# Performance work log

Measured on AMD Instinct MI355X. Metric: run time of the kernel, lower is better.

The kernel has to match this reference:

```python
import jax, jax.numpy as jnp
import numpy as np

B, N, C, H, DFF = 64, 196, 384, 8, 1536
PATCH = 14              # N == PATCH*PATCH, PATCH = image_size // 2
HD = C // H
SCALE = HD ** -0.5


def setup_inputs() -> dict:
    key = jax.random.key(0)
    ks = jax.random.split(key, 12)
    r = lambda i, shape: jax.random.normal(ks[i], shape, jnp.float32) * 0.02
    return dict(
        src=jax.random.normal(ks[0], (B, N, C), jnp.float32),
        src1=jax.random.normal(ks[1], (B, N, C), jnp.float32),
        ln_pre_g=jnp.ones((C,), jnp.float32), ln_pre_b=jnp.zeros((C,), jnp.float32),
        ln1_g=jnp.ones((C,), jnp.float32), ln1_b=jnp.zeros((C,), jnp.float32),
        wqkv_a=r(2, (C, 4 * C)), wproj_a=r(3, (C, C)), bproj_a=jnp.zeros((C,), jnp.float32),
        se_w1=r(4, (C, C // 16)), se_w2=r(5, (C // 16, C)),
        sa_w=r(6, (1, 2, 5, 5)), sa_b=jnp.zeros((1,), jnp.float32),
        wqkv_c=r(7, (C, 4 * C)), wproj_c=r(8, (C, C)), bproj_c=jnp.zeros((C,), jnp.float32),
        w1=r(9, (C, DFF)), b1=jnp.zeros((DFF,), jnp.float32),
        w2=r(10, (DFF, C)), b2=jnp.zeros((C,), jnp.float32),
    )


def _ln(x, g, b):
    m = x.mean(-1, keepdims=True)
    v = ((x - m) ** 2).mean(-1, keepdims=True)
    return (x - m) * jax.lax.rsqrt(v + 1e-5) * g + b


def _qkv4(x, w):
    b, n, _ = x.shape
    q = (x @ w).reshape(b, n, 4, H, HD).transpose(2, 0, 3, 1, 4)  # (4,B,H,N,hd)
    return q[0], q[1], q[2], q[3]


def _se(q, w1, w2):
    # SELayer: channel gate over (B, H*hd, N)
    b, h, n, c = q.shape
    xt = q.transpose(0, 1, 3, 2).reshape(b, h * c, n)
    fc = lambda v: jax.nn.sigmoid(jax.nn.relu(v @ w1) @ w2)
    gate = fc(xt.mean(-1)) + fc(xt.max(-1))
    xt = xt * gate[:, :, None]
    return xt.reshape(b, h, c, n).transpose(0, 1, 3, 2)


def _sa(q, w, bias):
    # SALayer: spatial gate via 5x5 conv on avg/max channel pooling
    b, h, n, c = q.shape
    xi = q.transpose(0, 1, 3, 2).reshape(b, h * c, PATCH, PATCH)
    pooled = jnp.concatenate([xi.mean(1, keepdims=True), xi.max(1, keepdims=True)], axis=1)
    conv = jax.lax.conv_general_dilated(pooled, w, (1, 1), [(2, 2), (2, 2)],
                                        dimension_numbers=('NCHW', 'OIHW', 'NCHW'))
    gate = jax.nn.sigmoid(conv + bias[None, :, None, None])
    xi = xi * gate
    return xi.reshape(b, h, c, n).transpose(0, 1, 3, 2)


def _merge(o):  # (B,H,N,hd) -> (B,N,C)
    return o.transpose(0, 2, 1, 3).reshape(o.shape[0], o.shape[2], C)


def _attention(x, y, wqkv, wproj, bproj, se_w1, se_w2, sa_w, sa_b):
    qxo, qx, kx, vx = _qkv4(x, wqkv)
    qyo, qy, ky, _ = _qkv4(y, wqkv)
    vy = vx  # original code: vy = qkv[3] (x-stream values)
    qx2 = _se(qx, se_w1, se_w2)
    qy2 = _sa(qy, sa_w, sa_b)
    a1 = jax.nn.softmax(jnp.einsum('bhqd,bhkd->bhqk', qx + qx2, kx) * SCALE, axis=-1)
    a2 = jax.nn.softmax(jnp.einsum('bhqd,bhkd->bhqk', qy + qy2, ky) * SCALE, axis=-1)
    xo = _merge(jnp.einsum('bhqk,bhkd->bhqd', a1, vx)) @ wproj + bproj
    yo = _merge(jnp.einsum('bhqk,bhkd->bhqd', a2, vy)) @ wproj + bproj
    # original overwrites cross outputs with proj(proj(.))
    return xo, yo, xo @ wproj + bproj, yo @ wproj + bproj


def _dif(x, y, wqkv, wproj, bproj):
    qxo, qx, kx, vx = _qkv4(x, wqkv)
    qyo, qy, ky, _ = _qkv4(y, wqkv)
    vy = vx
    a1 = jax.nn.softmax(jnp.einsum('bhqd,bhkd->bhqk', qx, kx) * SCALE, axis=-1)
    a2 = jax.nn.softmax(jnp.einsum('bhqd,bhkd->bhqk', qy, ky) * SCALE, axis=-1)
    ax = jax.nn.softmax(-jnp.einsum('bhqd,bhkd->bhqk', qyo, kx) * SCALE, axis=-1)
    ay = jax.nn.softmax(-jnp.einsum('bhqd,bhkd->bhqk', qxo, ky) * SCALE, axis=-1)
    xo = _merge(jnp.einsum('bhqk,bhkd->bhqd', a1, vx) + jnp.einsum('bhqk,bhkd->bhqd', ax, vx))
    yo = _merge(jnp.einsum('bhqk,bhkd->bhqd', a2, vy) + jnp.einsum('bhqk,bhkd->bhqd', ay, vy))
    return xo @ wproj + bproj, yo @ wproj + bproj


def _mlp(x, w1, b1, w2, b2):
    return jax.nn.gelu(x @ w1 + b1, approximate=False) @ w2 + b2


def reference(src, src1, ln_pre_g, ln_pre_b, ln1_g, ln1_b, wqkv_a, wproj_a, bproj_a,
              se_w1, se_w2, sa_w, sa_b, wqkv_c, wproj_c, bproj_c, w1, b1, w2, b2):
    x0, y0 = src, src1
    xa, ya, xoa, yoa = _attention(_ln(src, ln_pre_g, ln_pre_b), _ln(src1, ln_pre_g, ln_pre_b),
                                  wqkv_a, wproj_a, bproj_a, se_w1, se_w2, sa_w, sa_b)
    x = x0 + xa
    xo = x0 + xoa
    y = y0 + ya
    yo = y0 + yoa
    x, y, xo, yo = (_ln(t, ln1_g, ln1_b) for t in (x, y, xo, yo))
    x = x + _mlp(x, w1, b1, w2, b2)
    y = y + _mlp(y, w1, b1, w2, b2)
    xo = xo + _mlp(xo, w1, b1, w2, b2)
    yo = yo + _mlp(yo, w1, b1, w2, b2)
    # c_attn REPLACES the streams (no residual on attention itself)
    x, y = _dif(_ln(x, ln_pre_g, ln_pre_b), _ln(y, ln_pre_g, ln_pre_b), wqkv_c, wproj_c, bproj_c)
    x = x + _mlp(x, w1, b1, w2, b2)
    y = y + _mlp(y, w1, b1, w2, b2)
    return (x, y, xo, yo)
```

## Files before the change

### kernel.cpp

```cpp
#include <hip/hip_runtime.h>
#include <math.h>

#define Bb   64
#define Nn   196
#define Cc   384
#define Hh   8
#define HDd  48
#define DFFf 1536
#define MRr  (Bb * Nn)

typedef __attribute__((ext_vector_type(8))) short bf16x8v;
typedef __attribute__((ext_vector_type(4))) float f32x4v;

__device__ __forceinline__ ushort f2bf(float f){
  union { float f; uint u; } v; v.f = f;
  uint r = v.u + 0x7FFFu + ((v.u >> 16) & 1u);
  return (ushort)(r >> 16);
}
__device__ __forceinline__ float bf2f(ushort u){
  union { uint u; float f; } v; v.u = ((uint)u) << 16;
  return v.f;
}

__device__ __forceinline__ float wsum(float v){
#pragma unroll
  for (int o = 32; o; o >>= 1) v += __shfl_xor(v, o, 64);
  return v;
}
__device__ __forceinline__ float wmaxr(float v){
#pragma unroll
  for (int o = 32; o; o >>= 1) v = fmaxf(v, __shfl_xor(v, o, 64));
  return v;
}

__global__ void lnstats_k(const float* __restrict__ A, const float* __restrict__ A2,
                          float* __restrict__ m, float* __restrict__ rs){
  int row  = blockIdx.x;
  int lane = threadIdx.x;
  size_t base = (size_t)row * Cc;
  float x[6];
#pragma unroll
  for (int i = 0; i < 6; ++i){
    int c = lane + 64 * i;
    float v = A[base + c];
    if (A2) v += A2[base + c];
    x[i] = v;
  }
  float s = x[0] + x[1] + x[2] + x[3] + x[4] + x[5];
  s = wsum(s);
  float mm = s * (1.f / Cc);
  float vs = 0.f;
#pragma unroll
  for (int i = 0; i < 6; ++i){ float d = x[i] - mm; vs += d * d; }
  vs = wsum(vs);
  if (lane == 0){
    m[row]  = mm;
    rs[row] = rsqrtf(vs * (1.f / Cc) + 1e-5f);
  }
}

__global__ void wconv_k(const float* __restrict__ W, ushort* __restrict__ WT,
                        int K, int N){
  int idx = blockIdx.x * 256 + threadIdx.x;
  if (idx >= K * N) return;
  int k = idx / N, n = idx - k * N;
  WT[(size_t)n * K + k] = f2bf(W[idx]);
}

#define BMm 128
#define BNn 128
#define BKk 64
#define LDK 72

__global__ __launch_bounds__(256) void mgemm_k(
    const float* __restrict__ A, int lda, const float* __restrict__ A2,
    const float* __restrict__ stm, const float* __restrict__ strs,
    const float* __restrict__ ag,  const float* __restrict__ ab,
    const ushort* __restrict__ WT, int ldwt, const float* __restrict__ bias, int act,
    const float* __restrict__ res, int ldres,
    const float* __restrict__ r1, const float* __restrict__ r2,
    const float* __restrict__ rm, const float* __restrict__ rrs,
    const float* __restrict__ rg, const float* __restrict__ rb,
    float* __restrict__ out, int ldo, int M, int K, int N){
  __shared__ ushort As[BMm][LDK];
  __shared__ ushort Bs[BNn][LDK];
  const int tid  = threadIdx.x;
  const int lane = tid & 63;
  const int wid  = tid >> 6;
  const int wr = wid >> 1, wc = wid & 1;
  const int row0 = blockIdx.y * BMm;
  const int n0   = blockIdx.x * BNn;

  f32x4v acc[4][4];
#pragma unroll
  for (int m = 0; m < 4; ++m)
#pragma unroll
    for (int n = 0; n < 4; ++n) acc[m][n] = (f32x4v){0.f, 0.f, 0.f, 0.f};

  const int arow = tid >> 4;
  const int akq  = (tid & 15) * 4;
  const int bcol = tid >> 1;
  const int bko  = (tid & 1) * 32;

  for (int k0 = 0; k0 < K; k0 += BKk){
#pragma unroll
    for (int p = 0; p < 8; ++p){
      int r = arow + p * 16;
      int row = row0 + r;
      int kg = k0 + akq;
      float4 v = *(const float4*)&A[(size_t)row * lda + kg];
      if (A2){
        float4 w = *(const float4*)&A2[(size_t)row * lda + kg];
        v.x += w.x; v.y += w.y; v.z += w.z; v.w += w.w;
      }
      if (stm){
        float mm = stm[row], rr = strs[row];
        float4 g  = *(const float4*)&ag[kg];
        float4 bb = *(const float4*)&ab[kg];
        v.x = (v.x - mm) * rr * g.x + bb.x;
        v.y = (v.y - mm) * rr * g.y + bb.y;
        v.z = (v.z - mm) * rr * g.z + bb.z;
        v.w = (v.w - mm) * rr * g.w + bb.w;
      }
      ushort4 o; o.x = f2bf(v.x); o.y = f2bf(v.y); o.z = f2bf(v.z); o.w = f2bf(v.w);
      *(ushort4*)&As[r][akq] = o;
    }
    {
      const ushort* src = &WT[(size_t)(n0 + bcol) * ldwt + k0 + bko];
#pragma unroll
      for (int q = 0; q < 4; ++q)
        *(uint4*)&Bs[bcol][bko + q * 8] = *(const uint4*)(src + q * 8);
    }
    __syncthreads();
#pragma unroll
    for (int ks = 0; ks < 2; ++ks){
      const int kb = ks * 32 + (lane >> 4) * 8;
      bf16x8v af[4], bfm[4];
#pragma unroll
      for (int m = 0; m < 4; ++m)
        af[m] = *(const bf16x8v*)&As[wr * 64 + m * 16 + (lane & 15)][kb];
#pragma unroll
      for (int n = 0; n < 4; ++n)
        bfm[n] = *(const bf16x8v*)&Bs[wc * 64 + n * 16 + (lane & 15)][kb];
#pragma unroll
      for (int m = 0; m < 4; ++m)
#pragma unroll
        for (int n = 0; n < 4; ++n)
          acc[m][n] = __builtin_amdgcn_mfma_f32_16x16x32_bf16(af[m], bfm[n], acc[m][n], 0, 0, 0);
    }
    __syncthreads();
  }
  const int rbase = row0 + wr * 64 + (lane >> 4) * 4;
  const int cbase = n0 + wc * 64 + (lane & 15);
#pragma unroll
  for (int m = 0; m < 4; ++m){
#pragma unroll
    for (int n = 0; n < 4; ++n){
      int ccol = cbase + n * 16;
      float bv = bias ? bias[ccol] : 0.f;
#pragma unroll
      for (int j = 0; j < 4; ++j){
        int rr_ = rbase + m * 16 + j;
        float v = acc[m][n][j] + bv;
        if (act) v = 0.5f * v * (1.f + erff(v * 0.70710678118654752f));
        if (res) v += res[(size_t)rr_ * ldres + ccol];
        if (r1)  v += (r1[(size_t)rr_ * ldres + ccol] + r2[(size_t)rr_ * ldres + ccol]
                       - rm[rr_]) * rrs[rr_] * rg[ccol] + rb[ccol];
        out[(size_t)rr_ * ldo + ccol] = v;
      }
    }
  }
}

__global__ void se_k(const float* __restrict__ q, int rs_, const float* __restrict__ w1,
                     const float* __restrict__ w2, float* __restrict__ gate){
  int b = blockIdx.x;
  int tid = threadIdx.x;
  __shared__ float mv[Cc], xv[Cc], hid[2][24];
  for (int c = tid; c < Cc; c += 256){
    const float* p = q + (size_t)b * Nn * rs_ + c;
    float s = 0.f, mx = -INFINITY;
    for (int n = 0; n < Nn; ++n){
      float v = p[(size_t)n * rs_];
      s += v; mx = fmaxf(mx, v);
    }
    mv[c] = s * (1.f / Nn); xv[c] = mx;
  }
  __syncthreads();
  if (tid < 48){
    int vec = tid / 24, j = tid % 24;
    const float* v = vec ? xv : mv;
    float s = 0.f;
    for (int c = 0; c < Cc; ++c) s += v[c] * w1[c * 24 + j];
    hid[vec][j] = fmaxf(s, 0.f);
  }
  __syncthreads();
  for (int c = tid; c < Cc; c += 256){
    float s0 = 0.f, s1 = 0.f;
    for (int j = 0; j < 24; ++j){
      float w = w2[j * Cc + c];
      s0 += hid[0][j] * w; s1 += hid[1][j] * w;
    }
    gate[b * Cc + c] = 1.f + 1.f / (1.f + __expf(-s0)) + 1.f / (1.f + __expf(-s1));
  }
}

__global__ void sa_k(const float* __restrict__ q, int rs_, const float* __restrict__ w,
                     const float* __restrict__ bias, float* __restrict__ gate){
  int b = blockIdx.x;
  int tid = threadIdx.x;
  __shared__ float pm[Nn], px[Nn];
  if (tid < Nn){
    const float* p = q + ((size_t)b * Nn + tid) * rs_;
    float s = 0.f, mx = -INFINITY;
    for (int c = 0; c < Cc; ++c){ float v = p[c]; s += v; mx = fmaxf(mx, v); }
    pm[tid] = s * (1.f / Cc); px[tid] = mx;
  }
  __syncthreads();
  if (tid < Nn){
    int py = tid / 14, pxx = tid % 14;
    float acc = 0.f;
    for (int ky = 0; ky < 5; ++ky){
      int yy = py + ky - 2;
      if (yy < 0 || yy >= 14) continue;
      for (int kx = 0; kx < 5; ++kx){
        int xx = pxx + kx - 2;
        if (xx < 0 || xx >= 14) continue;
        int n2 = yy * 14 + xx;
        acc += pm[n2] * w[ky * 5 + kx] + px[n2] * w[25 + ky * 5 + kx];
      }
    }
    acc += bias[0];
    gate[b * Nn + tid] = 1.f + 1.f / (1.f + __expf(-acc));
  }
}

__global__ __launch_bounds__(512) void attn_k(
    const float* __restrict__ q1, int q1rs, float sg1,
    const float* __restrict__ q2, int q2rs, float sg2,
    const float* __restrict__ kp, int krs,
    const float* __restrict__ vp, int vrs,
    const float* __restrict__ gate_c, const float* __restrict__ gate_n,
    float* __restrict__ out){
  __shared__ float  Kt[HDd][256];
  __shared__ ushort Vb[Nn][HDd];
  __shared__ float  ql[8][HDd];
  __shared__ float  pl[8][200];
  int bh = blockIdx.x, b = bh >> 3, h = bh & 7;
  int tid = threadIdx.x, w = tid >> 6, lane = tid & 63;
  int hoff = h * HDd;
  for (int e = tid; e < 256 * HDd; e += 512){
    int n = e / HDd, d = e - n * HDd;
    float kv = 0.f;
    if (n < Nn){
      size_t rr = (size_t)b * Nn + n;
      kv = kp[rr * krs + hoff + d];
      Vb[n][d] = f2bf(vp[rr * vrs + hoff + d]);
    }
    Kt[d][n] = kv;
  }
  __syncthreads();
  int nstream = q2 ? 2 : 1;
  for (int r = w; r < Nn; r += 8){
    float oacc = 0.f;
    for (int st = 0; st < nstream; ++st){
      const float* qb = st ? q2 : q1;
      int rs_ = st ? q2rs : q1rs;
      float sg = st ? sg2 : sg1;
      if (lane < HDd){
        float qv = qb[((size_t)b * Nn + r) * rs_ + hoff + lane];
        if (st == 0){
          if (gate_c) qv *= gate_c[b * Cc + hoff + lane];
          if (gate_n) qv *= gate_n[b * Nn + r];
        }
        ql[w][lane] = qv * sg;
      }
      float sv0 = 0.f, sv1 = 0.f, sv2 = 0.f, sv3 = 0.f;
#pragma unroll 4
      for (int d = 0; d < HDd; ++d){
        float qd = ql[w][d];
        sv0 = fmaf(qd, Kt[d][lane      ], sv0);
        sv1 = fmaf(qd, Kt[d][lane +  64], sv1);
        sv2 = fmaf(qd, Kt[d][lane + 128], sv2);
        sv3 = fmaf(qd, Kt[d][lane + 192], sv3);
      }
      if (lane >= 4) sv3 = -INFINITY;
      float lmax = wmaxr(fmaxf(fmaxf(sv0, sv1), fmaxf(sv2, sv3)));
      float e0 = __expf(sv0 - lmax), e1 = __expf(sv1 - lmax), e2 = __expf(sv2 - lmax);
      float e3 = (lane < 4) ? __expf(sv3 - lmax) : 0.f;
      float lsum = wsum(e0 + e1 + e2 + e3);
      pl[w][lane] = e0; pl[w][lane + 64] = e1; pl[w][lane + 128] = e2;
      if (lane < 4) pl[w][lane + 192] = e3;
      float inv = 1.f / lsum;
      if (lane < HDd){
        float a2 = 0.f;
        for (int k = 0; k < Nn; k += 4){
          float4 p4 = *(const float4*)&pl[w][k];
          a2 = fmaf(p4.x, bf2f(Vb[k    ][lane]), a2);
          a2 = fmaf(p4.y, bf2f(Vb[k + 1][lane]), a2);
          a2 = fmaf(p4.z, bf2f(Vb[k + 2][lane]), a2);
          a2 = fmaf(p4.w, bf2f(Vb[k + 3][lane]), a2);
        }
        oacc += inv * a2;
      }
    }
    if (lane < HDd)
      out[((size_t)b * Nn + r) * Cc + hoff + lane] = oacc;
  }
}

extern "C" void kernel_launch(void* const* d_in, const int* in_sizes, int n_in,
                              void* d_out, int out_size, void* d_ws, size_t ws_size,
                              hipStream_t stream){
  const float* src    = (const float*)d_in[0];
  const float* src1   = (const float*)d_in[1];
  const float* lnpg   = (const float*)d_in[2];
  const float* lnpb   = (const float*)d_in[3];
  const float* ln1g   = (const float*)d_in[4];
  const float* ln1b   = (const float*)d_in[5];
  const float* wqkva  = (const float*)d_in[6];
  const float* wproja = (const float*)d_in[7];
  const float* bproja = (const float*)d_in[8];
  const float* sew1   = (const float*)d_in[9];
  const float* sew2   = (const float*)d_in[10];
  const float* saw    = (const float*)d_in[11];
  const float* sab    = (const float*)d_in[12];
  const float* wqkvc  = (const float*)d_in[13];
  const float* wprojc = (const float*)d_in[14];
  const float* bprojc = (const float*)d_in[15];
  const float* w1     = (const float*)d_in[16];
  const float* b1     = (const float*)d_in[17];
  const float* w2     = (const float*)d_in[18];
  const float* b2     = (const float*)d_in[19];
  float* out = (float*)d_out;

  const size_t F = (size_t)Bb * Nn * Cc;
  const int MR = MRr;
  const float SCALE = 0.14433756729740643f;

  float* ws   = (float*)d_ws;
  float* Qb   = ws;
  float* S1   = ws + 4 * F;
  float* S2   = ws + 5 * F;
  float* st1m = ws + 6 * F;  float* st1r = st1m + MR;
  float* st2m = st1m + 2 * (size_t)MR; float* st2r = st1m + 3 * (size_t)MR;
  float* gse  = st1m + 4 * (size_t)MR;
  float* gsa  = gse + (size_t)Bb * Cc;
  ushort* WTa  = (ushort*)(gsa + (size_t)Bb * Nn);
  ushort* WTc  = WTa + (size_t)1536 * 384;
  ushort* WTpa = WTc + (size_t)1536 * 384;
  ushort* WTpc = WTpa + (size_t)384 * 384;
  ushort* WT1  = WTpc + (size_t)384 * 384;
  ushort* WT2  = WT1 + (size_t)1536 * 384;

  float* OX  = out;
  float* OY  = out + F;
  float* OXO = out + 2 * F;
  float* OYO = out + 3 * F;

  dim3 blk(256);
#define G(N_) dim3((N_) / BNn, MRr / BMm)
  const float* Z = nullptr;

  wconv_k<<<(384 * 1536 + 255) / 256, blk, 0, stream>>>(wqkva, WTa, 384, 1536);
  wconv_k<<<(384 * 1536 + 255) / 256, blk, 0, stream>>>(wqkvc, WTc, 384, 1536);
  wconv_k<<<(384 * 384 + 255) / 256,  blk, 0, stream>>>(wproja, WTpa, 384, 384);
  wconv_k<<<(384 * 384 + 255) / 256,  blk, 0, stream>>>(wprojc, WTpc, 384, 384);
  wconv_k<<<(384 * 1536 + 255) / 256, blk, 0, stream>>>(w1, WT1, 384, 1536);
  wconv_k<<<(1536 * 384 + 255) / 256, blk, 0, stream>>>(w2, WT2, 1536, 384);

  lnstats_k<<<MR, 64, 0, stream>>>(src,  nullptr, st1m, st1r);
  lnstats_k<<<MR, 64, 0, stream>>>(src1, nullptr, st2m, st2r);
  mgemm_k<<<G(1152), blk, 0, stream>>>(src, Cc, Z, st1m, st1r, lnpg, lnpb,
      WTa + (size_t)384 * 384, 384, Z, 0, Z, 0, Z, Z, Z, Z, Z, Z, Qb, 1152, MR, Cc, 1152);
  mgemm_k<<<G(768), blk, 0, stream>>>(src1, Cc, Z, st2m, st2r, lnpg, lnpb,
      WTa + (size_t)384 * 384, 384, Z, 0, Z, 0, Z, Z, Z, Z, Z, Z, OXO, 768, MR, Cc, 768);
  se_k<<<Bb, 256, 0, stream>>>(Qb, 1152, sew1, sew2, gse);
  sa_k<<<Bb, 256, 0, stream>>>(OXO, 768, saw, sab, gsa);
  attn_k<<<Bb * Hh, 512, 0, stream>>>(Qb, 1152, SCALE, Z, 0, 0.f,
      Qb + 384, 1152, Qb + 768, 1152, gse, Z, OX);
  attn_k<<<Bb * Hh, 512, 0, stream>>>(OXO, 768, SCALE, Z, 0, 0.f,
      OXO + 384, 768, Qb + 768, 1152, Z, gsa, OY);
  mgemm_k<<<G(384), blk, 0, stream>>>(OX, Cc, Z, Z, Z, Z, Z, WTpa, 384, bproja, 0,
      Z, 0, Z, Z, Z, Z, Z, Z, S1, Cc, MR, Cc, Cc);
  mgemm_k<<<G(384), blk, 0, stream>>>(OY, Cc, Z, Z, Z, Z, Z, WTpa, 384, bproja, 0,
      Z, 0, Z, Z, Z, Z, Z, Z, S2, Cc, MR, Cc, Cc);
  mgemm_k<<<G(384), blk, 0, stream>>>(S1, Cc, Z, Z, Z, Z, Z, WTpa, 384, bproja, 0,
      Z, 0, Z, Z, Z, Z, Z, Z, OXO, Cc, MR, Cc, Cc);
  mgemm_k<<<G(384), blk, 0, stream>>>(S2, Cc, Z, Z, Z, Z, Z, WTpa, 384, bproja, 0,
      Z, 0, Z, Z, Z, Z, Z, Z, OYO, Cc, MR, Cc, Cc);
  lnstats_k<<<MR, 64, 0, stream>>>(S1, src, st1m, st1r);
  mgemm_k<<<G(1536), blk, 0, stream>>>(S1, Cc, src, st1m, st1r, ln1g, ln1b,
      WT1, 384, b1, 1, Z, 0, Z, Z, Z, Z, Z, Z, Qb, DFFf, MR, Cc, DFFf);
  mgemm_k<<<G(384), blk, 0, stream>>>(Qb, DFFf, Z, Z, Z, Z, Z, WT2, 1536, b2, 0,
      Z, Cc, S1, src, st1m, st1r, ln1g, ln1b, S1, Cc, MR, DFFf, Cc);
  lnstats_k<<<MR, 64, 0, stream>>>(S2, src1, st1m, st1r);
  mgemm_k<<<G(1536), blk, 0, stream>>>(S2, Cc, src1, st1m, st1r, ln1g, ln1b,
      WT1, 384, b1, 1, Z, 0, Z, Z, Z, Z, Z, Z, Qb, DFFf, MR, Cc, DFFf);
  mgemm_k<<<G(384), blk, 0, stream>>>(Qb, DFFf, Z, Z, Z, Z, Z, WT2, 1536, b2, 0,
      Z, Cc, S2, src1, st1m, st1r, ln1g, ln1b, S2, Cc, MR, DFFf, Cc);
  lnstats_k<<<MR, 64, 0, stream>>>(OXO, src, st1m, st1r);
  mgemm_k<<<G(1536), blk, 0, stream>>>(OXO, Cc, src, st1m, st1r, ln1g, ln1b,
      WT1, 384, b1, 1, Z, 0, Z, Z, Z, Z, Z, Z, Qb, DFFf, MR, Cc, DFFf);
  mgemm_k<<<G(384), blk, 0, stream>>>(Qb, DFFf, Z, Z, Z, Z, Z, WT2, 1536, b2, 0,
      Z, Cc, OXO, src, st1m, st1r, ln1g, ln1b, OXO, Cc, MR, DFFf, Cc);
  lnstats_k<<<MR, 64, 0, stream>>>(OYO, src1, st1m, st1r);
  mgemm_k<<<G(1536), blk, 0, stream>>>(OYO, Cc, src1, st1m, st1r, ln1g, ln1b,
      WT1, 384, b1, 1, Z, 0, Z, Z, Z, Z, Z, Z, Qb, DFFf, MR, Cc, DFFf);
  mgemm_k<<<G(384), blk, 0, stream>>>(Qb, DFFf, Z, Z, Z, Z, Z, WT2, 1536, b2, 0,
      Z, Cc, OYO, src1, st1m, st1r, ln1g, ln1b, OYO, Cc, MR, DFFf, Cc);

  lnstats_k<<<MR, 64, 0, stream>>>(S1, nullptr, st1m, st1r);
  mgemm_k<<<G(1536), blk, 0, stream>>>(S1, Cc, Z, st1m, st1r, lnpg, lnpb,
      WTc, 384, Z, 0, Z, 0, Z, Z, Z, Z, Z, Z, Qb, 1536, MR, Cc, 1536);
  lnstats_k<<<MR, 64, 0, stream>>>(S2, nullptr, st2m, st2r);
  mgemm_k<<<G(384), blk, 0, stream>>>(S2, Cc, Z, st2m, st2r, lnpg, lnpb,
      WTc, 384, Z, 0, Z, 0, Z, Z, Z, Z, Z, Z, S1, Cc, MR, Cc, Cc);
  attn_k<<<Bb * Hh, 512, 0, stream>>>(Qb + 384, 1536, SCALE, S1, Cc, -SCALE,
      Qb + 768, 1536, Qb + 1152, 1536, Z, Z, OX);
  mgemm_k<<<G(768), blk, 0, stream>>>(S2, Cc, Z, st2m, st2r, lnpg, lnpb,
      WTc + (size_t)384 * 384, 384, Z, 0, Z, 0, Z, Z, Z, Z, Z, Z, Qb + 384, 1536, MR, Cc, 768);
  attn_k<<<Bb * Hh, 512, 0, stream>>>(Qb + 384, 1536, SCALE, Qb, 1536, -SCALE,
      Qb + 768, 1536, Qb + 1152, 1536, Z, Z, OY);
  mgemm_k<<<G(384), blk, 0, stream>>>(OX, Cc, Z, Z, Z, Z, Z, WTpc, 384, bprojc, 0,
      Z, 0, Z, Z, Z, Z, Z, Z, S2, Cc, MR, Cc, Cc);
  mgemm_k<<<G(384), blk, 0, stream>>>(OY, Cc, Z, Z, Z, Z, Z, WTpc, 384, bprojc, 0,
      Z, 0, Z, Z, Z, Z, Z, Z, S1, Cc, MR, Cc, Cc);
  mgemm_k<<<G(1536), blk, 0, stream>>>(S2, Cc, Z, Z, Z, Z, Z,
      WT1, 384, b1, 1, Z, 0, Z, Z, Z, Z, Z, Z, Qb, DFFf, MR, Cc, DFFf);
  mgemm_k<<<G(384), blk, 0, stream>>>(Qb, DFFf, Z, Z, Z, Z, Z, WT2, 1536, b2, 0,
      S2, Cc, Z, Z, Z, Z, Z, Z, OX, Cc, MR, DFFf, Cc);
  mgemm_k<<<G(1536), blk, 0, stream>>>(S1, Cc, Z, Z, Z, Z, Z,
      WT1, 384, b1, 1, Z, 0, Z, Z, Z, Z, Z, Z, Qb, DFFf, MR, Cc, DFFf);
  mgemm_k<<<G(384), blk, 0, stream>>>(Qb, DFFf, Z, Z, Z, Z, Z, WT2, 1536, b2, 0,
      S1, Cc, Z, Z, Z, Z, Z, Z, OY, Cc, MR, DFFf, Cc);
#undef G
}
```

Measured before the change: 3.284 ms.

## Register-block attention over four query rows per wave with bf16 K and probabilities

The attention kernel now has each wave process four query rows at once. Every K and V value read from shared memory is reused across four rows instead of one. K and the softmax probabilities are stored as packed bf16 pairs, which halves their shared-memory footprint and read traffic, and blocks shrink from 512 to 256 threads. The cost is higher register pressure and extra bf16 rounding on K and the probabilities, which may affect accuracy.

```diff
diff --git a/kernel.cpp b/kernel.cpp
--- a/kernel.cpp
+++ b/kernel.cpp
@@ -20,6 +20,12 @@
 __device__ __forceinline__ float bf2f(ushort u){
   union { uint u; float f; } v; v.u = ((uint)u) << 16;
   return v.f;
+}
+__device__ __forceinline__ float ubf_lo(uint u){
+  union { uint u; float f; } v; v.u = u << 16; return v.f;
+}
+__device__ __forceinline__ float ubf_hi(uint u){
+  union { uint u; float f; } v; v.u = u & 0xffff0000u; return v.f;
 }
 
 __device__ __forceinline__ float wsum(float v){
@@ -235,21 +241,21 @@
   }
 }
 
-__global__ __launch_bounds__(512) void attn_k(
+__global__ __launch_bounds__(256) void attn_k(
     const float* __restrict__ q1, int q1rs, float sg1,
     const float* __restrict__ q2, int q2rs, float sg2,
     const float* __restrict__ kp, int krs,
     const float* __restrict__ vp, int vrs,
     const float* __restrict__ gate_c, const float* __restrict__ gate_n,
     float* __restrict__ out){
-  __shared__ float  Kt[HDd][256];
+  __shared__ ushort Ktb[HDd][256];
   __shared__ ushort Vb[Nn][HDd];
-  __shared__ float  ql[8][HDd];
-  __shared__ float  pl[8][200];
+  __shared__ float  ql[4][4][HDd];
+  __shared__ uint   plp[4][4][128];
   int bh = blockIdx.x, b = bh >> 3, h = bh & 7;
   int tid = threadIdx.x, w = tid >> 6, lane = tid & 63;
   int hoff = h * HDd;
-  for (int e = tid; e < 256 * HDd; e += 512){
+  for (int e = tid; e < 256 * HDd; e += 256){
     int n = e / HDd, d = e - n * HDd;
     float kv = 0.f;
     if (n < Nn){
@@ -257,55 +263,88 @@
       kv = kp[rr * krs + hoff + d];
       Vb[n][d] = f2bf(vp[rr * vrs + hoff + d]);
     }
-    Kt[d][n] = kv;
+    Ktb[d][n] = f2bf(kv);
   }
   __syncthreads();
+  const uint* kt32 = (const uint*)Ktb;
   int nstream = q2 ? 2 : 1;
-  for (int r = w; r < Nn; r += 8){
-    float oacc = 0.f;
+  const bool c23ok = (lane <= 33);
+  for (int g = w; g < 49; g += 4){
+    int r0 = g * 4;
+    float oacc[4] = {0.f, 0.f, 0.f, 0.f};
     for (int st = 0; st < nstream; ++st){
       const float* qb = st ? q2 : q1;
       int rs_ = st ? q2rs : q1rs;
       float sg = st ? sg2 : sg1;
       if (lane < HDd){
-        float qv = qb[((size_t)b * Nn + r) * rs_ + hoff + lane];
-        if (st == 0){
-          if (gate_c) qv *= gate_c[b * Cc + hoff + lane];
-          if (gate_n) qv *= gate_n[b * Nn + r];
+#pragma unroll
+        for (int ri = 0; ri < 4; ++ri){
+          int r = r0 + ri;
+          float qv = qb[((size_t)b * Nn + r) * rs_ + hoff + lane];
+          if (st == 0){
+            if (gate_c) qv *= gate_c[b * Cc + hoff + lane];
+            if (gate_n) qv *= gate_n[b * Nn + r];
+          }
+          ql[w][ri][lane] = qv * sg;
         }
-        ql[w][lane] = qv * sg;
-      }
-      float sv0 = 0.f, sv1 = 0.f, sv2 = 0.f, sv3 = 0.f;
-#pragma unroll 4
+      }
+      float sv[4][4];
+#pragma unroll
+      for (int ri = 0; ri < 4; ++ri){
+        sv[ri][0] = 0.f; sv[ri][1] = 0.f; sv[ri][2] = 0.f; sv[ri][3] = 0.f;
+      }
       for (int d = 0; d < HDd; ++d){
-        float qd = ql[w][d];
-        sv0 = fmaf(qd, Kt[d][lane      ], sv0);
-        sv1 = fmaf(qd, Kt[d][lane +  64], sv1);
-        sv2 = fmaf(qd, Kt[d][lane + 128], sv2);
-        sv3 = fmaf(qd, Kt[d][lane + 192], sv3);
-      }
-      if (lane >= 4) sv3 = -INFINITY;
-      float lmax = wmaxr(fmaxf(fmaxf(sv0, sv1), fmaxf(sv2, sv3)));
-      float e0 = __expf(sv0 - lmax), e1 = __expf(sv1 - lmax), e2 = __expf(sv2 - lmax);
-      float e3 = (lane < 4) ? __expf(sv3 - lmax) : 0.f;
-      float lsum = wsum(e0 + e1 + e2 + e3);
-      pl[w][lane] = e0; pl[w][lane + 64] = e1; pl[w][lane + 128] = e2;
-      if (lane < 4) pl[w][lane + 192] = e3;
-      float inv = 1.f / lsum;
+        uint ka  = kt32[d * 128 + lane];
+        uint kbp = kt32[d * 128 + 64 + lane];
+        float kA0 = ubf_lo(ka),  kA1 = ubf_hi(ka);
+        float kB0 = ubf_lo(kbp), kB1 = ubf_hi(kbp);
+        float q0 = ql[w][0][d], q1v = ql[w][1][d];
+        float q2v = ql[w][2][d], q3v = ql[w][3][d];
+        sv[0][0] = fmaf(q0, kA0, sv[0][0]); sv[0][1] = fmaf(q0, kA1, sv[0][1]);
+        sv[0][2] = fmaf(q0, kB0, sv[0][2]); sv[0][3] = fmaf(q0, kB1, sv[0][3]);
+        sv[1][0] = fmaf(q1v, kA0, sv[1][0]); sv[1][1] = fmaf(q1v, kA1, sv[1][1]);
+        sv[1][2] = fmaf(q1v, kB0, sv[1][2]); sv[1][3] = fmaf(q1v, kB1, sv[1][3]);
+        sv[2][0] = fmaf(q2v, kA0, sv[2][0]); sv[2][1] = fmaf(q2v, kA1, sv[2][1]);
+        sv[2][2] = fmaf(q2v, kB0, sv[2][2]); sv[2][3] = fmaf(q2v, kB1, sv[2][3]);
+        sv[3][0] = fmaf(q3v, kA0, sv[3][0]); sv[3][1] = fmaf(q3v, kA1, sv[3][1]);
+        sv[3][2] = fmaf(q3v, kB0, sv[3][2]); sv[3][3] = fmaf(q3v, kB1, sv[3][3]);
+      }
+      float inv[4];
+#pragma unroll
+      for (int ri = 0; ri < 4; ++ri){
+        float m01 = fmaxf(sv[ri][0], sv[ri][1]);
+        float m23 = c23ok ? fmaxf(sv[ri][2], sv[ri][3]) : -INFINITY;
+        float m = wmaxr(fmaxf(m01, m23));
+        float e0 = __expf(sv[ri][0] - m);
+        float e1 = __expf(sv[ri][1] - m);
+        float e2 = c23ok ? __expf(sv[ri][2] - m) : 0.f;
+        float e3 = c23ok ? __expf(sv[ri][3] - m) : 0.f;
+        float ls = wsum(e0 + e1 + e2 + e3);
+        inv[ri] = 1.f / ls;
+        plp[w][ri][lane]      = ((uint)f2bf(e0)) | (((uint)f2bf(e1)) << 16);
+        plp[w][ri][64 + lane] = ((uint)f2bf(e2)) | (((uint)f2bf(e3)) << 16);
+      }
       if (lane < HDd){
-        float a2 = 0.f;
-        for (int k = 0; k < Nn; k += 4){
-          float4 p4 = *(const float4*)&pl[w][k];
-          a2 = fmaf(p4.x, bf2f(Vb[k    ][lane]), a2);
-          a2 = fmaf(p4.y, bf2f(Vb[k + 1][lane]), a2);
-          a2 = fmaf(p4.z, bf2f(Vb[k + 2][lane]), a2);
-          a2 = fmaf(p4.w, bf2f(Vb[k + 3][lane]), a2);
+        float a0 = 0.f, a1 = 0.f, a2 = 0.f, a3 = 0.f;
+        for (int j = 0; j < 98; ++j){
+          float v0 = bf2f(Vb[2 * j][lane]);
+          float v1 = bf2f(Vb[2 * j + 1][lane]);
+          uint p0 = plp[w][0][j], p1 = plp[w][1][j];
+          uint p2 = plp[w][2][j], p3 = plp[w][3][j];
+          a0 = fmaf(ubf_lo(p0), v0, a0); a0 = fmaf(ubf_hi(p0), v1, a0);
+          a1 = fmaf(ubf_lo(p1), v0, a1); a1 = fmaf(ubf_hi(p1), v1, a1);
+          a2 = fmaf(ubf_lo(p2), v0, a2); a2 = fmaf(ubf_hi(p2), v1, a2);
+          a3 = fmaf(ubf_lo(p3), v0, a3); a3 = fmaf(ubf_hi(p3), v1, a3);
         }
-        oacc += inv * a2;
-      }
-    }
-    if (lane < HDd)
-      out[((size_t)b * Nn + r) * Cc + hoff + lane] = oacc;
+        oacc[0] += inv[0] * a0; oacc[1] += inv[1] * a1;
+        oacc[2] += inv[2] * a2; oacc[3] += inv[3] * a3;
+      }
+    }
+    if (lane < HDd){
+#pragma unroll
+      for (int ri = 0; ri < 4; ++ri)
+        out[((size_t)b * Nn + r0 + ri) * Cc + hoff + lane] = oacc[ri];
+    }
   }
 }
 
@@ -377,9 +416,9 @@
       WTa + (size_t)384 * 384, 384, Z, 0, Z, 0, Z, Z, Z, Z, Z, Z, OXO, 768, MR, Cc, 768);
   se_k<<<Bb, 256, 0, stream>>>(Qb, 1152, sew1, sew2, gse);
   sa_k<<<Bb, 256, 0, stream>>>(OXO, 768, saw, sab, gsa);
-  attn_k<<<Bb * Hh, 512, 0, stream>>>(Qb, 1152, SCALE, Z, 0, 0.f,
+  attn_k<<<Bb * Hh, 256, 0, stream>>>(Qb, 1152, SCALE, Z, 0, 0.f,
       Qb + 384, 1152, Qb + 768, 1152, gse, Z, OX);
-  attn_k<<<Bb * Hh, 512, 0, stream>>>(OXO, 768, SCALE, Z, 0, 0.f,
+  attn_k<<<Bb * Hh, 256, 0, stream>>>(OXO, 768, SCALE, Z, 0, 0.f,
       OXO + 384, 768, Qb + 768, 1152, Z, gsa, OY);
   mgemm_k<<<G(384), blk, 0, stream>>>(OX, Cc, Z, Z, Z, Z, Z, WTpa, 384, bproja, 0,
       Z, 0, Z, Z, Z, Z, Z, Z, S1, Cc, MR, Cc, Cc);
@@ -416,11 +455,11 @@
   lnstats_k<<<MR, 64, 0, stream>>>(S2, nullptr, st2m, st2r);
   mgemm_k<<<G(384), blk, 0, stream>>>(S2, Cc, Z, st2m, st2r, lnpg, lnpb,
       WTc, 384, Z, 0, Z, 0, Z, Z, Z, Z, Z, Z, S1, Cc, MR, Cc, Cc);
-  attn_k<<<Bb * Hh, 512, 0, stream>>>(Qb + 384, 1536, SCALE, S1, Cc, -SCALE,
+  attn_k<<<Bb * Hh, 256, 0, stream>>>(Qb + 384, 1536, SCALE, S1, Cc, -SCALE,
       Qb + 768, 1536, Qb + 1152, 1536, Z, Z, OX);
   mgemm_k<<<G(768), blk, 0, stream>>>(S2, Cc, Z, st2m, st2r, lnpg, lnpb,
       WTc + (size_t)384 * 384, 384, Z, 0, Z, 0, Z, Z, Z, Z, Z, Z, Qb + 384, 1536, MR, Cc, 768);
-  attn_k<<<Bb * Hh, 512, 0, stream>>>(Qb + 384, 1536, SCALE, Qb, 1536, -SCALE,
+  attn_k<<<Bb * Hh, 256, 0, stream>>>(Qb + 384, 1536, SCALE, Qb, 1536, -SCALE,
       Qb + 768, 1536, Qb + 1152, 1536, Z, Z, OY);
   mgemm_k<<<G(384), blk, 0, stream>>>(OX, Cc, Z, Z, Z, Z, Z, WTpc, 384, bprojc, 0,
       Z, 0, Z, Z, Z, Z, Z, Z, S2, Cc, MR, Cc, Cc);
```

Result: faster. 2.835 ms (-13.7%).
